# Performance work log

Measured on AMD Instinct MI355X. Metric: run time of the kernel, lower is better.

Reference implementation:

```python
import jax, jax.numpy as jnp
import numpy as np

CFG = {"dt": 1.0, "T_r": 2.0, "kappa_j": 1.0, "tau_j": 10.0, "gamma_m": 1.0, "R_m": 1.0,
       "tau_m": 20.0, "thresh": 1.0, "tau_tr": 20.0, "tau_data": 10.0,
       "alpha_gen": 0.5, "alpha_disc": 0.5}


def _lif(v, x, tr, j, refrac, ti, cfg):
    """One LIF update for a hidden layer (bPC_SNNLayer.update_state)."""
    dt = cfg["dt"]
    j = j + dt / cfg["tau_j"] * (-cfg["kappa_j"] * j + ti)
    is_refr = refrac > 0
    v_next = v + dt / cfg["tau_m"] * (-cfg["gamma_m"] * v + cfg["R_m"] * j)
    v = jnp.where(is_refr, v, v_next)
    spikes = (v > cfg["thresh"]).astype(v.dtype) * (1.0 - is_refr.astype(v.dtype))
    v = v * (1.0 - spikes)
    refrac = jnp.maximum(refrac - dt, 0.0)
    refrac = jnp.where(spikes > 0, jnp.asarray(cfg["T_r"], v.dtype), refrac)
    tr = tr - tr / cfg["tau_tr"] + spikes  # spike trace (layer.x)
    return v, spikes, tr, j, refrac


def _forward(x_data, y_target, W0, W1, W2, V0, V1, V2, num_steps):
    cfg = CFG
    B = x_data.shape[0]
    d0, d1, d2, d3 = x_data.shape[1], W0.shape[1], W1.shape[1], W2.shape[1]
    dt_ = x_data.dtype
    z = lambda d: jnp.zeros((B, d), dt_)
    state = dict(v1=z(d1), tr1=z(d1), j1=z(d1), r1=z(d1), s1=z(d1),
                 v2=z(d2), tr2=z(d2), j2=z(d2), r2=z(d2), s2=z(d2),
                 eg0=z(d0), eg1=z(d1), eg2=z(d2),
                 ed1=z(d1), ed2=z(d2), ed3=z(d3),
                 z_data=z(d0), z_label=z(d3))
    ag, ad = cfg["alpha_gen"], cfg["alpha_disc"]

    def step(st, _):
        # phase 1: currents into hidden layers 1 and 2 (layers 0/3 are data/label, no-op)
        ti1 = -st["eg1"] + st["ed2"] @ V1 - st["ed1"] + st["eg0"] @ W0
        ti2 = -st["eg2"] + st["ed3"] @ V2 - st["ed2"] + st["eg1"] @ W1
        v1, s1, tr1, j1, r1 = _lif(st["v1"], st["tr1"], st["tr1"], st["j1"], st["r1"], ti1, cfg) if False else _lif(st["v1"], st["tr1"], st["tr1"], st["j1"], st["r1"], ti1, cfg)
        v1, s1, tr1, j1, r1 = _lif(st["v1"], st["tr1"], st["tr1"], st["j1"], st["r1"], ti1, cfg)
        v2, s2, tr2, j2, r2 = _lif(st["v2"], st["tr2"], st["tr2"], st["j2"], st["r2"], ti2, cfg)
        # phase 2: error recomputation (training mode with label clamped)
        z_data = st["z_data"] - st["z_data"] / cfg["tau_data"] + x_data
        z_label = st["z_label"] - st["z_label"] / cfg["tau_data"] + y_target
        eg0 = ag * (z_data - s1 @ W0.T)          # layer 0 generative error
        ed1 = ad * (tr1 - x_data @ V0.T)          # layer 1 discriminative error
        eg1 = ag * (tr1 - s2 @ W1.T)
        ed2 = ad * (tr2 - s1 @ V1.T)
        eg2 = ag * (tr2 - y_target @ W2.T)        # top hidden: label-clamped generative target
        ed3 = ad * (z_label - s2 @ V2.T)          # label layer discriminative error
        return dict(v1=v1, tr1=tr1, j1=j1, r1=r1, s1=s1,
                    v2=v2, tr2=tr2, j2=j2, r2=r2, s2=s2,
                    eg0=eg0, eg1=eg1, eg2=eg2, ed1=ed1, ed2=ed2, ed3=ed3,
                    z_data=z_data, z_label=z_label), None

    final, _ = jax.lax.scan(step, state, None, length=num_steps)
    return final["ed3"]


def setup_inputs() -> dict:
    key = jax.random.key(0)
    ks = jax.random.split(key, 8)
    B = 128
    sizes = (2048, 4096, 4096, 512)
    sc = 0.02  # weight scale kept small so dynamics stay numerically sane over 16 steps
    return {
        "x_data": jax.random.normal(ks[0], (B, sizes[0]), jnp.float32),
        "y_target": jax.random.normal(ks[1], (B, sizes[3]), jnp.float32),
        "W0": jax.random.normal(ks[2], (sizes[0], sizes[1]), jnp.float32) * sc,
        "W1": jax.random.normal(ks[3], (sizes[1], sizes[2]), jnp.float32) * sc,
        "W2": jax.random.normal(ks[4], (sizes[2], sizes[3]), jnp.float32) * sc,
        "V0": jax.random.normal(ks[5], (sizes[1], sizes[0]), jnp.float32) * sc,
        "V1": jax.random.normal(ks[6], (sizes[2], sizes[1]), jnp.float32) * sc,
        "V2": jax.random.normal(ks[7], (sizes[3], sizes[2]), jnp.float32) * sc,
        "num_steps": 16,
    }


def reference(x_data, y_target, W0, W1, W2, V0, V1, V2, num_steps):
    return _forward(x_data, y_target, W0, W1, W2, V0, V1, V2, num_steps)
```

## Files before the change

### kernel.cpp

```cpp
#include <hip/hip_runtime.h>


#define DEVINL __device__ __forceinline__

using bf16x8 = __attribute__((ext_vector_type(8))) __bf16;
using f32x4  = __attribute__((ext_vector_type(4))) float;
using i32x4  = __attribute__((ext_vector_type(4))) int;
typedef unsigned char uchar;

static constexpr int BB = 128;
static constexpr int D0 = 2048, D1 = 4096, D2 = 4096, D3 = 512;
static constexpr int NSTEPS = 16;

struct Ctx {
  const float *x, *y, *W0, *W1, *W2, *V0, *V1, *V2;
  float *v1, *j1, *r1, *tr1, *v2, *j2, *r2, *tr2;
  float *zd, *zl, *xV0T, *yW2T;
  __bf16 *x_bf, *y_bf, *eg0_bf, *eg1_bf, *ed2_bf, *ed3_bf;
  uchar *s1_f8, *s2_f8, *WA8, *WB8;
  __bf16 *W0t, *W1t, *V1t, *V2t, *V0n, *W2n;
  float *out;
};

DEVINL void gload16(const void* g, void* l) {
  __builtin_amdgcn_global_load_lds(
      (const __attribute__((address_space(1))) void*)g,
      (__attribute__((address_space(3))) void*)l, 16, 0, 0);
}
DEVINL uint32_t lds_off(const void* p) {
  return (uint32_t)(uintptr_t)(__attribute__((address_space(3))) const void*)p;
}
DEVINL bf16x8 dsr128(uint32_t addr) {
  i32x4 r;
  asm volatile("ds_read_b128 %0, %1" : "=v"(r) : "v"(addr));
  return __builtin_bit_cast(bf16x8, r);
}
DEVINL long dsr64(uint32_t addr) {
  long r;
  asm volatile("ds_read_b64 %0, %1" : "=v"(r) : "v"(addr));
  return r;
}

struct Seg { const __bf16* A; unsigned ldA; const __bf16* W; unsigned ldW; int iters; };
struct SPtr { const __bf16 *a0, *a1, *w; };
struct SPtrW { const __bf16 *a, *w; };

DEVINL SPtr mkptr(const Seg& s, int t) {
  int r = t >> 3;
  int u = ((t & 7) ^ (r & 7)) * 8;
  SPtr p;
  p.a0 = s.A + (size_t)r * s.ldA + u;
  p.a1 = s.A + (size_t)(r + 32) * s.ldA + u;
  p.w  = s.W + (size_t)r * s.ldW + u;
  return p;
}
DEVINL SPtrW mkptrw(const Seg& s, int t) {
  int r = t >> 3;
  int u = ((t & 7) ^ (r & 7)) * 8;
  SPtrW p;
  p.a = s.A + (size_t)r * s.ldA + u;
  p.w = s.W + (size_t)r * s.ldW + u;
  return p;
}

DEVINL void run_gemm(const Seg* segs, int nIter, __bf16* lsA, __bf16* lsW,
                     int t, int wm, int wn, int l16, int lg, f32x4* acc) {
  const int seg0it = segs[0].iters;
  SPtr p = mkptr(segs[0], t);
  int nxt = 0;
  auto stage = [&](int s) {
    __bf16* bA = lsA + (s & 3) * 4096;
    __bf16* bW = lsW + (s & 3) * 2048;
    gload16(p.a0, bA + t * 8);
    gload16(p.a1, bA + 2048 + t * 8);
    gload16(p.w,  bW + t * 8);
    p.a0 += 64; p.a1 += 64; p.w += 64;
    if (++nxt == seg0it) p = mkptr(segs[1], t);
  };

  const int x7 = l16 & 7;
  uint32_t aB = lds_off(lsA), wB = lds_off(lsW);
  uint32_t aAd[2][2], wAd[2];
#pragma unroll
  for (int mt = 0; mt < 2; ++mt)
#pragma unroll
    for (int ks = 0; ks < 2; ++ks)
      aAd[mt][ks] = aB + (uint32_t)(wm * 32 + mt * 16 + l16) * 128u
                       + (uint32_t)(((ks * 4 + lg) ^ x7) * 16);
#pragma unroll
  for (int ks = 0; ks < 2; ++ks)
    wAd[ks] = wB + (uint32_t)(wn * 16 + l16) * 128u
                 + (uint32_t)(((ks * 4 + lg) ^ x7) * 16);

  auto compute = [&](int i) {
    uint32_t oa = (uint32_t)(i & 3) * 8192u, ow = (uint32_t)(i & 3) * 4096u;
    bf16x8 a00 = dsr128(aAd[0][0] + oa);
    bf16x8 a01 = dsr128(aAd[0][1] + oa);
    bf16x8 a10 = dsr128(aAd[1][0] + oa);
    bf16x8 a11 = dsr128(aAd[1][1] + oa);
    bf16x8 b0  = dsr128(wAd[0] + ow);
    bf16x8 b1  = dsr128(wAd[1] + ow);
    asm volatile("s_waitcnt lgkmcnt(0)" ::: "memory");
    __builtin_amdgcn_sched_barrier(0);
    __builtin_amdgcn_s_setprio(1);
    acc[0] = __builtin_amdgcn_mfma_f32_16x16x32_bf16(a00, b0, acc[0], 0, 0, 0);
    acc[1] = __builtin_amdgcn_mfma_f32_16x16x32_bf16(a10, b0, acc[1], 0, 0, 0);
    acc[0] = __builtin_amdgcn_mfma_f32_16x16x32_bf16(a01, b1, acc[0], 0, 0, 0);
    acc[1] = __builtin_amdgcn_mfma_f32_16x16x32_bf16(a11, b1, acc[1], 0, 0, 0);
    __builtin_amdgcn_s_setprio(0);
  };

  stage(0); stage(1); stage(2);
  for (int i = 0; i < nIter - 3; ++i) {
    asm volatile("s_waitcnt vmcnt(6)" ::: "memory");
    __builtin_amdgcn_s_barrier();
    stage(i + 3);
    compute(i);
  }
  asm volatile("s_waitcnt vmcnt(6)" ::: "memory");
  __builtin_amdgcn_s_barrier();
  compute(nIter - 3);
  asm volatile("s_waitcnt vmcnt(3)" ::: "memory");
  __builtin_amdgcn_s_barrier();
  compute(nIter - 2);
  asm volatile("s_waitcnt vmcnt(0)" ::: "memory");
  __builtin_amdgcn_s_barrier();
  compute(nIter - 1);
}

DEVINL void run_gemm128w(const Seg* segs, int nIter, __bf16* lsA, __bf16* lsW,
                         int t, int wm, int wn, int l16, int lg, f32x4* acc) {
  const int seg0it = segs[0].iters;
  SPtrW p = mkptrw(segs[0], t);
  int nxt = 0;
  auto stage = [&](int buf) {
    __bf16* bA = lsA + buf * 8192;
    __bf16* bW = lsW + buf * 8192;
    gload16(p.a,      bA + t * 8);
    gload16(p.a + 64, bA + 4096 + t * 8);
    gload16(p.w,      bW + t * 8);
    gload16(p.w + 64, bW + 4096 + t * 8);
    p.a += 128; p.w += 128;
    if (++nxt == seg0it) p = mkptrw(segs[1], t);
  };

  const int x7 = l16 & 7;
  uint32_t aB = lds_off(lsA), wB = lds_off(lsW);
  uint32_t aAd[2][2], wAd[2];
#pragma unroll
  for (int mt = 0; mt < 2; ++mt)
#pragma unroll
    for (int ks = 0; ks < 2; ++ks)
      aAd[mt][ks] = aB + (uint32_t)(wm * 32 + mt * 16 + l16) * 128u
                       + (uint32_t)(((ks * 4 + lg) ^ x7) * 16);
#pragma unroll
  for (int ks = 0; ks < 2; ++ks)
    wAd[ks] = wB + (uint32_t)(wn * 16 + l16) * 128u
                 + (uint32_t)(((ks * 4 + lg) ^ x7) * 16);

  auto compute = [&](int buf) {
    uint32_t oa = (uint32_t)buf * 16384u, ow = (uint32_t)buf * 16384u;
    bf16x8 a00 = dsr128(aAd[0][0] + oa);
    bf16x8 a01 = dsr128(aAd[0][1] + oa);
    bf16x8 a10 = dsr128(aAd[1][0] + oa);
    bf16x8 a11 = dsr128(aAd[1][1] + oa);
    bf16x8 b0  = dsr128(wAd[0] + ow);
    bf16x8 b1  = dsr128(wAd[1] + ow);
    bf16x8 c00 = dsr128(aAd[0][0] + oa + 8192);
    bf16x8 c01 = dsr128(aAd[0][1] + oa + 8192);
    bf16x8 c10 = dsr128(aAd[1][0] + oa + 8192);
    bf16x8 c11 = dsr128(aAd[1][1] + oa + 8192);
    bf16x8 d0  = dsr128(wAd[0] + ow + 8192);
    bf16x8 d1  = dsr128(wAd[1] + ow + 8192);
    asm volatile("s_waitcnt lgkmcnt(0)" ::: "memory");
    __builtin_amdgcn_sched_barrier(0);
    __builtin_amdgcn_s_setprio(1);
    acc[0] = __builtin_amdgcn_mfma_f32_16x16x32_bf16(a00, b0, acc[0], 0, 0, 0);
    acc[1] = __builtin_amdgcn_mfma_f32_16x16x32_bf16(a10, b0, acc[1], 0, 0, 0);
    acc[0] = __builtin_amdgcn_mfma_f32_16x16x32_bf16(a01, b1, acc[0], 0, 0, 0);
    acc[1] = __builtin_amdgcn_mfma_f32_16x16x32_bf16(a11, b1, acc[1], 0, 0, 0);
    acc[0] = __builtin_amdgcn_mfma_f32_16x16x32_bf16(c00, d0, acc[0], 0, 0, 0);
    acc[1] = __builtin_amdgcn_mfma_f32_16x16x32_bf16(c10, d0, acc[1], 0, 0, 0);
    acc[0] = __builtin_amdgcn_mfma_f32_16x16x32_bf16(c01, d1, acc[0], 0, 0, 0);
    acc[1] = __builtin_amdgcn_mfma_f32_16x16x32_bf16(c11, d1, acc[1], 0, 0, 0);
    __builtin_amdgcn_s_setprio(0);
  };

  stage(0); stage(1);
  int cur = 0, nx = 2;
  for (int i = 0; i < nIter - 2; ++i) {
    asm volatile("s_waitcnt vmcnt(4)" ::: "memory");
    __builtin_amdgcn_s_barrier();
    stage(nx);
    compute(cur);
    cur = (cur == 2) ? 0 : cur + 1;
    nx  = (nx == 2) ? 0 : nx + 1;
  }
  asm volatile("s_waitcnt vmcnt(4)" ::: "memory");
  __builtin_amdgcn_s_barrier();
  compute(cur);
  cur = (cur == 2) ? 0 : cur + 1;
  asm volatile("s_waitcnt vmcnt(0)" ::: "memory");
  __builtin_amdgcn_s_barrier();
  compute(cur);
}


__global__ __launch_bounds__(512, 1) void phase1_v17(Ctx c, float edsc) {
  __shared__ __align__(16) __bf16 lsA[3][8192];
  __shared__ __align__(16) __bf16 lsW[3][8192];
  int t = threadIdx.x, w = t >> 6, l = t & 63;
  int l16 = l & 15, lg = l >> 4, wm = w >> 2, wn = w & 3;
  int bx = blockIdx.x;
  int z = bx >> 7, idx = bx & 127;
  int mh = idx >> 6, n0 = (idx & 63) * 64;
  f32x4 acc[2];
  f32x4 z4 = {0.f, 0.f, 0.f, 0.f};
  acc[0] = z4; acc[1] = z4;

  Seg segs[2]; int nIter, N;
  float *v, *j, *rf, *tr; const float* aux; const __bf16* buf; uchar* sf8;
  if (z == 0) {
    segs[0] = { c.ed2_bf + (size_t)mh * 64 * D2, (unsigned)D2, c.V1t + (size_t)n0 * D2, (unsigned)D2, 32 };
    segs[1] = { c.eg0_bf + (size_t)mh * 64 * D0, (unsigned)D0, c.W0t + (size_t)n0 * D0, (unsigned)D0, 16 };
    nIter = 48; N = D1;
    v = c.v1; j = c.j1; rf = c.r1; tr = c.tr1; buf = c.eg1_bf; aux = c.xV0T; sf8 = c.s1_f8;
  } else {
    segs[0] = { c.ed3_bf + (size_t)mh * 64 * D3, (unsigned)D3, c.V2t + (size_t)n0 * D3, (unsigned)D3, 4 };
    segs[1] = { c.eg1_bf + (size_t)mh * 64 * D1, (unsigned)D1, c.W1t + (size_t)n0 * D1, (unsigned)D1, 32 };
    nIter = 36; N = D2;
    v = c.v2; j = c.j2; rf = c.r2; tr = c.tr2; buf = c.ed2_bf; aux = c.yW2T; sf8 = c.s2_f8;
  }

  run_gemm128w(segs, nIter, &lsA[0][0], &lsW[0][0], t, wm, wn, l16, lg, acc);

  int n = n0 + wn * 16 + l16;
#pragma unroll
  for (int mt = 0; mt < 2; ++mt) {
#pragma unroll
    for (int r = 0; r < 4; ++r) {
      int b = mh * 64 + wm * 32 + mt * 16 + lg * 4 + r;
      size_t idx2 = (size_t)b * N + n;
      float to = tr[idx2];
      float ti = acc[mt][r] - (float)buf[idx2] - edsc * (to - aux[idx2]);
      float jo = j[idx2];
      float jn = jo + 0.1f * (ti - jo);
      float ro = rf[idx2];
      float vo = v[idx2];
      bool refr = ro > 0.0f;
      float vn = refr ? vo : (vo + 0.05f * (jn - vo));
      float sp = (!refr && vn > 1.0f) ? 1.0f : 0.0f;
      if (sp != 0.0f) vn = 0.0f;
      float rn = fmaxf(ro - 1.0f, 0.0f);
      if (sp != 0.0f) rn = 2.0f;
      float tn = to - 0.05f * to + sp;
      v[idx2] = vn; j[idx2] = jn; rf[idx2] = rn; tr[idx2] = tn;
      sf8[idx2] = (sp != 0.0f) ? (uchar)0x38 : (uchar)0;
    }
  }
}


__global__ __launch_bounds__(512, 2) void phase2_v18(Ctx c) {
  __shared__ __align__(128) uchar lsA[4][8192];
  __shared__ __align__(128) uchar lsW[4][8192];
  int t = threadIdx.x, w = t >> 6, l = t & 63;
  int l16 = l & 15, lg = l >> 4, wm = w >> 2, wn = w & 3;
  int g = blockIdx.x, mh = blockIdx.y;

  const uchar *A, *W; int n0; bool isA;
  if (g < 96) { isA = true;  A = c.s1_f8 + (size_t)mh * 64 * D1; W = c.WA8 + (size_t)g * 64 * 4096;        n0 = g * 64; }
  else        { isA = false; A = c.s2_f8 + (size_t)mh * 64 * D2; W = c.WB8 + (size_t)(g - 96) * 64 * 4096; n0 = (g - 96) * 64; }

  f32x4 acc[2];
  f32x4 z4 = {0.f, 0.f, 0.f, 0.f};
  acc[0] = z4; acc[1] = z4;

  int row8 = t >> 3, u8 = t & 7;
  int su8 = (u8 ^ ((row8 >> 1) & 7)) * 16;
  const uchar* pA = A + (size_t)row8 * 4096 + su8;
  const uchar* pW = W + (size_t)row8 * 4096 + su8;
  uchar* dA = &lsA[0][0] + t * 16;
  uchar* dW = &lsW[0][0] + t * 16;
  auto stage = [&](int s) {
    uint32_t o = (uint32_t)(s & 3) * 8192u;
    gload16(pA, dA + o);
    gload16(pW, dW + o);
    pA += 128; pW += 128;
  };

  uint32_t aB = lds_off(lsA), wB = lds_off(lsW);
  uint32_t adA[2], adW;
#pragma unroll
  for (int mt = 0; mt < 2; ++mt) {
    int ra = wm * 32 + mt * 16 + l16;
    adA[mt] = aB + (uint32_t)ra * 128u
            + (uint32_t)((((lg >> 1) ^ ((ra >> 1) & 7)) * 16) + (lg & 1) * 8);
  }
  {
    int rw = wn * 16 + l16;
    adW = wB + (uint32_t)rw * 128u
        + (uint32_t)((((lg >> 1) ^ ((rw >> 1) & 7)) * 16) + (lg & 1) * 8);
  }

  auto compute = [&](int i) {
    uint32_t off = (uint32_t)(i & 3) * 8192u;
    uint32_t A0 = adA[0] + off, A1 = adA[1] + off, B0 = adW + off;
    long a0v0 = dsr64(A0);         long a1v0 = dsr64(A1);
    long b0v0 = dsr64(B0);
    long a0v1 = dsr64(A0 ^ 32u);   long a1v1 = dsr64(A1 ^ 32u);
    long b0v1 = dsr64(B0 ^ 32u);
    long a0v2 = dsr64(A0 ^ 64u);   long a1v2 = dsr64(A1 ^ 64u);
    long b0v2 = dsr64(B0 ^ 64u);
    long a0v3 = dsr64(A0 ^ 96u);   long a1v3 = dsr64(A1 ^ 96u);
    long b0v3 = dsr64(B0 ^ 96u);
    asm volatile("s_waitcnt lgkmcnt(0)" ::: "memory");
    __builtin_amdgcn_sched_barrier(0);
    __builtin_amdgcn_s_setprio(1);
    acc[0] = __builtin_amdgcn_mfma_f32_16x16x32_fp8_fp8(a0v0, b0v0, acc[0], 0, 0, 0);
    acc[1] = __builtin_amdgcn_mfma_f32_16x16x32_fp8_fp8(a1v0, b0v0, acc[1], 0, 0, 0);
    acc[0] = __builtin_amdgcn_mfma_f32_16x16x32_fp8_fp8(a0v1, b0v1, acc[0], 0, 0, 0);
    acc[1] = __builtin_amdgcn_mfma_f32_16x16x32_fp8_fp8(a1v1, b0v1, acc[1], 0, 0, 0);
    acc[0] = __builtin_amdgcn_mfma_f32_16x16x32_fp8_fp8(a0v2, b0v2, acc[0], 0, 0, 0);
    acc[1] = __builtin_amdgcn_mfma_f32_16x16x32_fp8_fp8(a1v2, b0v2, acc[1], 0, 0, 0);
    acc[0] = __builtin_amdgcn_mfma_f32_16x16x32_fp8_fp8(a0v3, b0v3, acc[0], 0, 0, 0);
    acc[1] = __builtin_amdgcn_mfma_f32_16x16x32_fp8_fp8(a1v3, b0v3, acc[1], 0, 0, 0);
    __builtin_amdgcn_s_setprio(0);
  };

  const int nIter = 32;
  stage(0); stage(1); stage(2);
  for (int i = 0; i < nIter - 3; ++i) {
    asm volatile("s_waitcnt vmcnt(4)" ::: "memory");
    __builtin_amdgcn_s_barrier();
    stage(i + 3);
    compute(i);
  }
  asm volatile("s_waitcnt vmcnt(4)" ::: "memory");
  __builtin_amdgcn_s_barrier();
  compute(nIter - 3);
  asm volatile("s_waitcnt vmcnt(2)" ::: "memory");
  __builtin_amdgcn_s_barrier();
  compute(nIter - 2);
  asm volatile("s_waitcnt vmcnt(0)" ::: "memory");
  __builtin_amdgcn_s_barrier();
  compute(nIter - 1);

#pragma unroll
  for (int mt = 0; mt < 2; ++mt) {
    int nn = n0 + wn * 16 + l16;
#pragma unroll
    for (int r = 0; r < 4; ++r) {
      int b = mh * 64 + wm * 32 + mt * 16 + lg * 4 + r;
      float av = acc[mt][r];
      if (isA) {
        if (nn < 2048) {
          size_t idx = (size_t)b * D0 + nn;
          float zo = c.zd[idx]; float zn = zo - 0.1f * zo + c.x[idx];
          c.zd[idx] = zn;
          c.eg0_bf[idx] = (__bf16)(0.5f * (zn - av));
        } else {
          size_t idx = (size_t)b * D2 + (nn - 2048);
          c.ed2_bf[idx] = (__bf16)(0.5f * (c.tr2[idx] - av));
        }
      } else {
        if (nn < 4096) {
          size_t idx = (size_t)b * D1 + nn;
          c.eg1_bf[idx] = (__bf16)(0.5f * (c.tr1[idx] - av));
        } else {
          size_t idx = (size_t)b * D3 + (nn - 4096);
          float zo = c.zl[idx]; float zn = zo - 0.1f * zo + c.y[idx];
          c.zl[idx] = zn;
          float e = 0.5f * (zn - av);
          c.out[idx] = e; c.ed3_bf[idx] = (__bf16)e;
        }
      }
    }
  }
}


__global__ __launch_bounds__(256, 2) void precomp_v6(Ctx c) {
  __shared__ __align__(16) __bf16 lsA[4][4096];
  __shared__ __align__(16) __bf16 lsW[4][2048];
  int t = threadIdx.x, w = t >> 6, l = t & 63;
  int l16 = l & 15, lg = l >> 4, wm = w >> 1, wn = w & 1;
  int n0 = blockIdx.x * 32, mh = blockIdx.y;
  f32x4 acc[2];
  f32x4 z4 = {0.f, 0.f, 0.f, 0.f};
  acc[0] = z4; acc[1] = z4;

  Seg segs[2]; int nIter, N; float* outp;
  if (blockIdx.z == 0) {
    segs[0] = { c.x_bf + (size_t)mh * 64 * D0, (unsigned)D0, c.V0n + (size_t)n0 * D0, (unsigned)D0, 32 };
    nIter = 32; N = D1; outp = c.xV0T;
  } else {
    segs[0] = { c.y_bf + (size_t)mh * 64 * D3, (unsigned)D3, c.W2n + (size_t)n0 * D3, (unsigned)D3, 8 };
    nIter = 8; N = D2; outp = c.yW2T;
  }
  segs[1] = segs[0];

  run_gemm(segs, nIter, &lsA[0][0], &lsW[0][0], t, wm, wn, l16, lg, acc);

  int n = n0 + wn * 16 + l16;
#pragma unroll
  for (int mt = 0; mt < 2; ++mt)
#pragma unroll
    for (int r = 0; r < 4; ++r) {
      int b = mh * 64 + wm * 32 + mt * 16 + lg * 4 + r;
      outp[(size_t)b * N + n] = acc[mt][r];
    }
}


__global__ __launch_bounds__(256) void wprep_kernel(Ctx c, int g0) {
  __shared__ float ls[2][64][65];
  int g = blockIdx.x + g0;
  const float* src; __bf16* tp = nullptr; uchar* n8 = nullptr; __bf16* nb = nullptr; int R, C;
  if (g < 1024)       { src = c.W0; n8 = c.WA8;                         tp = c.W0t; R = D0; C = D1; }
  else if (g < 3072)  { g -= 1024;  src = c.W1; n8 = c.WB8;             tp = c.W1t; R = D1; C = D2; }
  else if (g < 5120)  { g -= 3072;  src = c.V1; n8 = c.WA8 + (size_t)2048 * 4096; tp = c.V1t; R = D2; C = D1; }
  else if (g < 5376)  { g -= 5120;  src = c.V2; n8 = c.WB8 + (size_t)4096 * 4096; tp = c.V2t; R = D3; C = D2; }
  else if (g < 6400)  { g -= 5376;  src = c.V0; nb = c.V0n; R = D1; C = D0; }
  else                { g -= 6400;  src = c.W2; nb = c.W2n; R = D2; C = D3; }
  int tpr = C / 128;
  int r0 = (g / tpr) * 64, c0 = (g % tpr) * 128;
  int t = threadIdx.x, r = t >> 2, q = t & 3;

  const float* base = src + (size_t)(r0 + r) * C + c0 + q * 16;
  float4 vv[2][4];
#pragma unroll
  for (int h = 0; h < 2; ++h)
#pragma unroll
    for (int i = 0; i < 4; ++i)
      vv[h][i] = reinterpret_cast<const float4*>(base + h * 64)[i];

  if (n8) {
#pragma unroll
    for (int h = 0; h < 2; ++h) {
      int pk[4];
#pragma unroll
      for (int i = 0; i < 4; i++) {
        float4 v = vv[h][i];
        ls[h][r][q * 16 + i * 4 + 0] = v.x; ls[h][r][q * 16 + i * 4 + 1] = v.y;
        ls[h][r][q * 16 + i * 4 + 2] = v.z; ls[h][r][q * 16 + i * 4 + 3] = v.w;
        int wd = __builtin_amdgcn_cvt_pk_fp8_f32(v.x, v.y, 0, false);
        wd = __builtin_amdgcn_cvt_pk_fp8_f32(v.z, v.w, wd, true);
        pk[i] = wd;
      }
      int4 pv; pv.x = pk[0]; pv.y = pk[1]; pv.z = pk[2]; pv.w = pk[3];
      *reinterpret_cast<int4*>(n8 + (size_t)(r0 + r) * C + c0 + h * 64 + q * 16) = pv;
    }
    __syncthreads();
#pragma unroll
    for (int h = 0; h < 2; ++h) {
      union { __bf16 hx[16]; int4 qq[2]; } wv;
#pragma unroll
      for (int i = 0; i < 16; i++) wv.hx[i] = (__bf16)ls[h][q * 16 + i][r];
      int4* dt = reinterpret_cast<int4*>(tp + (size_t)(c0 + h * 64 + r) * R + r0 + q * 16);
      dt[0] = wv.qq[0]; dt[1] = wv.qq[1];
    }
  } else {
#pragma unroll
    for (int h = 0; h < 2; ++h) {
      union { __bf16 hx[16]; int4 qq[2]; } uu;
#pragma unroll
      for (int i = 0; i < 4; i++) {
        float4 v = vv[h][i];
        uu.hx[i * 4 + 0] = (__bf16)v.x; uu.hx[i * 4 + 1] = (__bf16)v.y;
        uu.hx[i * 4 + 2] = (__bf16)v.z; uu.hx[i * 4 + 3] = (__bf16)v.w;
      }
      int4* dn = reinterpret_cast<int4*>(nb + (size_t)(r0 + r) * C + c0 + h * 64 + q * 16);
      dn[0] = uu.qq[0]; dn[1] = uu.qq[1];
    }
  }
}

__global__ __launch_bounds__(256) void castinit_kernel(Ctx c) {
  int i = blockIdx.x * 256 + threadIdx.x;
  const int NX = BB * D0 / 4;
  union { __bf16 h[4]; uint2 u; } p, q;
  if (i < NX) {
    float4 xv = reinterpret_cast<const float4*>(c.x)[i];
    reinterpret_cast<float4*>(c.zd)[i] = xv;
    p.h[0] = (__bf16)xv.x; p.h[1] = (__bf16)xv.y; p.h[2] = (__bf16)xv.z; p.h[3] = (__bf16)xv.w;
    reinterpret_cast<uint2*>(c.x_bf)[i] = p.u;
    q.h[0] = (__bf16)(0.5f * xv.x); q.h[1] = (__bf16)(0.5f * xv.y);
    q.h[2] = (__bf16)(0.5f * xv.z); q.h[3] = (__bf16)(0.5f * xv.w);
    reinterpret_cast<uint2*>(c.eg0_bf)[i] = q.u;
  } else {
    int k = i - NX;
    float4 yv = reinterpret_cast<const float4*>(c.y)[k];
    reinterpret_cast<float4*>(c.zl)[k] = yv;
    p.h[0] = (__bf16)yv.x; p.h[1] = (__bf16)yv.y; p.h[2] = (__bf16)yv.z; p.h[3] = (__bf16)yv.w;
    reinterpret_cast<uint2*>(c.y_bf)[k] = p.u;
    q.h[0] = (__bf16)(0.5f * yv.x); q.h[1] = (__bf16)(0.5f * yv.y);
    q.h[2] = (__bf16)(0.5f * yv.z); q.h[3] = (__bf16)(0.5f * yv.w);
    reinterpret_cast<uint2*>(c.ed3_bf)[k] = q.u;
  }
}


extern "C" void kernel_launch(void* const* d_in, const int* in_sizes, int n_in,
                              void* d_out, int out_size, void* d_ws, size_t ws_size,
                              hipStream_t stream) {
  Ctx c;
  c.x  = (const float*)d_in[0];
  c.y  = (const float*)d_in[1];
  c.W0 = (const float*)d_in[2];
  c.W1 = (const float*)d_in[3];
  c.W2 = (const float*)d_in[4];
  c.V0 = (const float*)d_in[5];
  c.V1 = (const float*)d_in[6];
  c.V2 = (const float*)d_in[7];
  c.out = (float*)d_out;

  char* p = (char*)d_ws;
  auto af = [&](size_t n) -> float* { float* r = (float*)p; p += ((n * 4 + 255) & ~(size_t)255); return r; };
  auto ah = [&](size_t n) -> __bf16* { __bf16* r = (__bf16*)p; p += ((n * 2 + 255) & ~(size_t)255); return r; };
  auto au = [&](size_t n) -> uchar* { uchar* r = (uchar*)p; p += ((n + 255) & ~(size_t)255); return r; };

  const size_t S1 = (size_t)BB * D1;
  c.v1 = af(S1); c.j1 = af(S1); c.r1 = af(S1); c.tr1 = af(S1);
  c.v2 = af(S1); c.j2 = af(S1); c.r2 = af(S1); c.tr2 = af(S1);
  c.eg1_bf = ah(S1); c.ed2_bf = ah(S1);
  size_t zero_bytes = (size_t)(p - (char*)d_ws);
  c.zd = af((size_t)BB * D0); c.zl = af((size_t)BB * D3);
  c.xV0T = af(S1); c.yW2T = af(S1);
  c.x_bf = ah((size_t)BB * D0); c.y_bf = ah((size_t)BB * D3);
  c.eg0_bf = ah((size_t)BB * D0); c.ed3_bf = ah((size_t)BB * D3);
  c.s1_f8 = au(S1); c.s2_f8 = au(S1);
  c.W0t = ah((size_t)D0 * D1); c.W1t = ah((size_t)D1 * D2); c.V1t = ah((size_t)D2 * D1); c.V2t = ah((size_t)D3 * D2);
  c.V0n = ah((size_t)D1 * D0); c.W2n = ah((size_t)D2 * D3);
  c.WA8 = au((size_t)(D0 + D2) * 4096);
  c.WB8 = au((size_t)(D1 + D3) * 4096);

  hipMemsetAsync(d_ws, 0, zero_bytes, stream);
  castinit_kernel<<<320, 256, 0, stream>>>(c);
  wprep_kernel<<<1536, 256, 0, stream>>>(c, 5120);
  wprep_kernel<<<2048, 256, 0, stream>>>(c, 1024);
  wprep_kernel<<<2048, 256, 0, stream>>>(c, 3072);
  wprep_kernel<<<1024, 256, 0, stream>>>(c, 0);
  precomp_v6<<<dim3(128, 2, 2), 256, 0, stream>>>(c);

  for (int s = 1; s < NSTEPS; s++) {
    phase1_v17<<<256, 512, 0, stream>>>(c, 0.5f);
    phase2_v18<<<dim3(168, 2), 512, 0, stream>>>(c);
  }
}
```

Measured before the change: 790.8 us.

## Store phase-1 transposed weights as fp8 and upconvert to bf16 in registers

The phase-1 GEMM now streams its transposed weight operands (W0t, W1t, V1t, V2t) as fp8 bytes instead of bf16. The weight-prep kernel writes fp8 transposes, the LDS weight buffer shrinks to bytes, and each wave reads 64-bit chunks and converts them to bf16 before the bf16 MFMAs. This halves weight global-memory traffic and LDS footprint in the memory-bound phase-1 kernel. It adds per-iteration conversion ALU work and loses weight precision, which may change the numerical results.

```diff
diff --git a/kernel.cpp b/kernel.cpp
--- a/kernel.cpp
+++ b/kernel.cpp
@@ -5,6 +5,7 @@
 
 using bf16x8 = __attribute__((ext_vector_type(8))) __bf16;
 using f32x4  = __attribute__((ext_vector_type(4))) float;
+using f32x2  = __attribute__((ext_vector_type(2))) float;
 using i32x4  = __attribute__((ext_vector_type(4))) int;
 typedef unsigned char uchar;
 
@@ -18,7 +19,8 @@
   float *zd, *zl, *xV0T, *yW2T;
   __bf16 *x_bf, *y_bf, *eg0_bf, *eg1_bf, *ed2_bf, *ed3_bf;
   uchar *s1_f8, *s2_f8, *WA8, *WB8;
-  __bf16 *W0t, *W1t, *V1t, *V2t, *V0n, *W2n;
+  uchar *W0t8, *W1t8, *V1t8, *V2t8;
+  __bf16 *V0n, *W2n;
   float *out;
 };
 
@@ -40,10 +42,25 @@
   asm volatile("ds_read_b64 %0, %1" : "=v"(r) : "v"(addr));
   return r;
 }
+DEVINL bf16x8 cvtw(long v) {
+  int lo = (int)(v & 0xffffffffL);
+  int hi = (int)(((unsigned long long)v) >> 32);
+  f32x2 p0 = __builtin_amdgcn_cvt_pk_f32_fp8(lo, false);
+  f32x2 p1 = __builtin_amdgcn_cvt_pk_f32_fp8(lo, true);
+  f32x2 p2 = __builtin_amdgcn_cvt_pk_f32_fp8(hi, false);
+  f32x2 p3 = __builtin_amdgcn_cvt_pk_f32_fp8(hi, true);
+  bf16x8 r;
+  r[0] = (__bf16)p0[0]; r[1] = (__bf16)p0[1];
+  r[2] = (__bf16)p1[0]; r[3] = (__bf16)p1[1];
+  r[4] = (__bf16)p2[0]; r[5] = (__bf16)p2[1];
+  r[6] = (__bf16)p3[0]; r[7] = (__bf16)p3[1];
+  return r;
+}
 
 struct Seg { const __bf16* A; unsigned ldA; const __bf16* W; unsigned ldW; int iters; };
 struct SPtr { const __bf16 *a0, *a1, *w; };
-struct SPtrW { const __bf16 *a, *w; };
+struct Seg8 { const __bf16* A; unsigned ldA; const uchar* W; unsigned ldW; int iters; };
+struct SP8 { const __bf16* a; const uchar* w; };
 
 DEVINL SPtr mkptr(const Seg& s, int t) {
   int r = t >> 3;
@@ -54,12 +71,13 @@
   p.w  = s.W + (size_t)r * s.ldW + u;
   return p;
 }
-DEVINL SPtrW mkptrw(const Seg& s, int t) {
+DEVINL SP8 mkptr8(const Seg8& s, int t) {
   int r = t >> 3;
-  int u = ((t & 7) ^ (r & 7)) * 8;
-  SPtrW p;
-  p.a = s.A + (size_t)r * s.ldA + u;
-  p.w = s.W + (size_t)r * s.ldW + u;
+  int ue = ((t & 7) ^ (r & 7)) * 8;
+  int ub = ((t & 7) ^ (r & 7)) * 16;
+  SP8 p;
+  p.a = s.A + (size_t)r * s.ldA + ue;
+  p.w = s.W + (size_t)r * s.ldW + ub;
   return p;
 }
 
@@ -128,52 +146,62 @@
   compute(nIter - 1);
 }
 
-DEVINL void run_gemm128w(const Seg* segs, int nIter, __bf16* lsA, __bf16* lsW,
-                         int t, int wm, int wn, int l16, int lg, f32x4* acc) {
+DEVINL void run_gemm128w8(const Seg8* segs, int nIter, __bf16* lsA, uchar* lsW8,
+                          int t, int wm, int wn, int l16, int lg, f32x4* acc) {
   const int seg0it = segs[0].iters;
-  SPtrW p = mkptrw(segs[0], t);
+  SP8 p = mkptr8(segs[0], t);
   int nxt = 0;
   auto stage = [&](int buf) {
     __bf16* bA = lsA + buf * 8192;
-    __bf16* bW = lsW + buf * 8192;
+    uchar*  bW = lsW8 + buf * 8192;
     gload16(p.a,      bA + t * 8);
     gload16(p.a + 64, bA + 4096 + t * 8);
-    gload16(p.w,      bW + t * 8);
-    gload16(p.w + 64, bW + 4096 + t * 8);
+    gload16(p.w,      bW + t * 16);
     p.a += 128; p.w += 128;
-    if (++nxt == seg0it) p = mkptrw(segs[1], t);
+    if (++nxt == seg0it) p = mkptr8(segs[1], t);
   };
 
   const int x7 = l16 & 7;
-  uint32_t aB = lds_off(lsA), wB = lds_off(lsW);
-  uint32_t aAd[2][2], wAd[2];
+  uint32_t aB = lds_off(lsA), wB = lds_off(lsW8);
+  uint32_t aAd[2][2], wAd8[2][2];
 #pragma unroll
   for (int mt = 0; mt < 2; ++mt)
 #pragma unroll
     for (int ks = 0; ks < 2; ++ks)
       aAd[mt][ks] = aB + (uint32_t)(wm * 32 + mt * 16 + l16) * 128u
                        + (uint32_t)(((ks * 4 + lg) ^ x7) * 16);
-#pragma unroll
-  for (int ks = 0; ks < 2; ++ks)
-    wAd[ks] = wB + (uint32_t)(wn * 16 + l16) * 128u
-                 + (uint32_t)(((ks * 4 + lg) ^ x7) * 16);
+  {
+    int rw = wn * 16 + l16;
+#pragma unroll
+    for (int h = 0; h < 2; ++h)
+#pragma unroll
+      for (int ks = 0; ks < 2; ++ks) {
+        int j = h * 4 + ks * 2 + (lg >> 1);
+        wAd8[h][ks] = wB + (uint32_t)rw * 128u
+                    + (uint32_t)(((j ^ (rw & 7)) * 16) + (lg & 1) * 8);
+      }
+  }
 
   auto compute = [&](int buf) {
-    uint32_t oa = (uint32_t)buf * 16384u, ow = (uint32_t)buf * 16384u;
+    uint32_t oa = (uint32_t)buf * 16384u, ow = (uint32_t)buf * 8192u;
     bf16x8 a00 = dsr128(aAd[0][0] + oa);
     bf16x8 a01 = dsr128(aAd[0][1] + oa);
     bf16x8 a10 = dsr128(aAd[1][0] + oa);
     bf16x8 a11 = dsr128(aAd[1][1] + oa);
-    bf16x8 b0  = dsr128(wAd[0] + ow);
-    bf16x8 b1  = dsr128(wAd[1] + ow);
     bf16x8 c00 = dsr128(aAd[0][0] + oa + 8192);
     bf16x8 c01 = dsr128(aAd[0][1] + oa + 8192);
     bf16x8 c10 = dsr128(aAd[1][0] + oa + 8192);
     bf16x8 c11 = dsr128(aAd[1][1] + oa + 8192);
-    bf16x8 d0  = dsr128(wAd[0] + ow + 8192);
-    bf16x8 d1  = dsr128(wAd[1] + ow + 8192);
+    long w00 = dsr64(wAd8[0][0] + ow);
+    long w01 = dsr64(wAd8[0][1] + ow);
+    long w10 = dsr64(wAd8[1][0] + ow);
+    long w11 = dsr64(wAd8[1][1] + ow);
     asm volatile("s_waitcnt lgkmcnt(0)" ::: "memory");
     __builtin_amdgcn_sched_barrier(0);
+    bf16x8 b0 = cvtw(w00);
+    bf16x8 b1 = cvtw(w01);
+    bf16x8 d0 = cvtw(w10);
+    bf16x8 d1 = cvtw(w11);
     __builtin_amdgcn_s_setprio(1);
     acc[0] = __builtin_amdgcn_mfma_f32_16x16x32_bf16(a00, b0, acc[0], 0, 0, 0);
     acc[1] = __builtin_amdgcn_mfma_f32_16x16x32_bf16(a10, b0, acc[1], 0, 0, 0);
@@ -189,14 +217,14 @@
   stage(0); stage(1);
   int cur = 0, nx = 2;
   for (int i = 0; i < nIter - 2; ++i) {
-    asm volatile("s_waitcnt vmcnt(4)" ::: "memory");
+    asm volatile("s_waitcnt vmcnt(3)" ::: "memory");
     __builtin_amdgcn_s_barrier();
     stage(nx);
     compute(cur);
     cur = (cur == 2) ? 0 : cur + 1;
     nx  = (nx == 2) ? 0 : nx + 1;
   }
-  asm volatile("s_waitcnt vmcnt(4)" ::: "memory");
+  asm volatile("s_waitcnt vmcnt(3)" ::: "memory");
   __builtin_amdgcn_s_barrier();
   compute(cur);
   cur = (cur == 2) ? 0 : cur + 1;
@@ -206,9 +234,9 @@
 }
 
 
-__global__ __launch_bounds__(512, 1) void phase1_v17(Ctx c, float edsc) {
+__global__ __launch_bounds__(512, 1) void phase1_v21(Ctx c, float edsc) {
   __shared__ __align__(16) __bf16 lsA[3][8192];
-  __shared__ __align__(16) __bf16 lsW[3][8192];
+  __shared__ __align__(128) uchar lsW8[3][8192];
   int t = threadIdx.x, w = t >> 6, l = t & 63;
   int l16 = l & 15, lg = l >> 4, wm = w >> 2, wn = w & 3;
   int bx = blockIdx.x;
@@ -218,21 +246,21 @@
   f32x4 z4 = {0.f, 0.f, 0.f, 0.f};
   acc[0] = z4; acc[1] = z4;
 
-  Seg segs[2]; int nIter, N;
+  Seg8 segs[2]; int nIter, N;
   float *v, *j, *rf, *tr; const float* aux; const __bf16* buf; uchar* sf8;
   if (z == 0) {
-    segs[0] = { c.ed2_bf + (size_t)mh * 64 * D2, (unsigned)D2, c.V1t + (size_t)n0 * D2, (unsigned)D2, 32 };
-    segs[1] = { c.eg0_bf + (size_t)mh * 64 * D0, (unsigned)D0, c.W0t + (size_t)n0 * D0, (unsigned)D0, 16 };
+    segs[0] = { c.ed2_bf + (size_t)mh * 64 * D2, (unsigned)D2, c.V1t8 + (size_t)n0 * D2, (unsigned)D2, 32 };
+    segs[1] = { c.eg0_bf + (size_t)mh * 64 * D0, (unsigned)D0, c.W0t8 + (size_t)n0 * D0, (unsigned)D0, 16 };
     nIter = 48; N = D1;
     v = c.v1; j = c.j1; rf = c.r1; tr = c.tr1; buf = c.eg1_bf; aux = c.xV0T; sf8 = c.s1_f8;
   } else {
-    segs[0] = { c.ed3_bf + (size_t)mh * 64 * D3, (unsigned)D3, c.V2t + (size_t)n0 * D3, (unsigned)D3, 4 };
-    segs[1] = { c.eg1_bf + (size_t)mh * 64 * D1, (unsigned)D1, c.W1t + (size_t)n0 * D1, (unsigned)D1, 32 };
+    segs[0] = { c.ed3_bf + (size_t)mh * 64 * D3, (unsigned)D3, c.V2t8 + (size_t)n0 * D3, (unsigned)D3, 4 };
+    segs[1] = { c.eg1_bf + (size_t)mh * 64 * D1, (unsigned)D1, c.W1t8 + (size_t)n0 * D1, (unsigned)D1, 32 };
     nIter = 36; N = D2;
     v = c.v2; j = c.j2; rf = c.r2; tr = c.tr2; buf = c.ed2_bf; aux = c.yW2T; sf8 = c.s2_f8;
   }
 
-  run_gemm128w(segs, nIter, &lsA[0][0], &lsW[0][0], t, wm, wn, l16, lg, acc);
+  run_gemm128w8(segs, nIter, &lsA[0][0], &lsW8[0][0], t, wm, wn, l16, lg, acc);
 
   int n = n0 + wn * 16 + l16;
 #pragma unroll
@@ -416,11 +444,11 @@
 __global__ __launch_bounds__(256) void wprep_kernel(Ctx c, int g0) {
   __shared__ float ls[2][64][65];
   int g = blockIdx.x + g0;
-  const float* src; __bf16* tp = nullptr; uchar* n8 = nullptr; __bf16* nb = nullptr; int R, C;
-  if (g < 1024)       { src = c.W0; n8 = c.WA8;                         tp = c.W0t; R = D0; C = D1; }
-  else if (g < 3072)  { g -= 1024;  src = c.W1; n8 = c.WB8;             tp = c.W1t; R = D1; C = D2; }
-  else if (g < 5120)  { g -= 3072;  src = c.V1; n8 = c.WA8 + (size_t)2048 * 4096; tp = c.V1t; R = D2; C = D1; }
-  else if (g < 5376)  { g -= 5120;  src = c.V2; n8 = c.WB8 + (size_t)4096 * 4096; tp = c.V2t; R = D3; C = D2; }
+  const float* src; uchar* t8 = nullptr; uchar* n8 = nullptr; __bf16* nb = nullptr; int R, C;
+  if (g < 1024)       { src = c.W0; n8 = c.WA8;                         t8 = c.W0t8; R = D0; C = D1; }
+  else if (g < 3072)  { g -= 1024;  src = c.W1; n8 = c.WB8;             t8 = c.W1t8; R = D1; C = D2; }
+  else if (g < 5120)  { g -= 3072;  src = c.V1; n8 = c.WA8 + (size_t)2048 * 4096; t8 = c.V1t8; R = D2; C = D1; }
+  else if (g < 5376)  { g -= 5120;  src = c.V2; n8 = c.WB8 + (size_t)4096 * 4096; t8 = c.V2t8; R = D3; C = D2; }
   else if (g < 6400)  { g -= 5376;  src = c.V0; nb = c.V0n; R = D1; C = D0; }
   else                { g -= 6400;  src = c.W2; nb = c.W2n; R = D2; C = D3; }
   int tpr = C / 128;
@@ -454,11 +482,19 @@
     __syncthreads();
 #pragma unroll
     for (int h = 0; h < 2; ++h) {
-      union { __bf16 hx[16]; int4 qq[2]; } wv;
-#pragma unroll
-      for (int i = 0; i < 16; i++) wv.hx[i] = (__bf16)ls[h][q * 16 + i][r];
-      int4* dt = reinterpret_cast<int4*>(tp + (size_t)(c0 + h * 64 + r) * R + r0 + q * 16);
-      dt[0] = wv.qq[0]; dt[1] = wv.qq[1];
+      int pk[4];
+#pragma unroll
+      for (int i = 0; i < 4; i++) {
+        float f0 = ls[h][q * 16 + i * 4 + 0][r];
+        float f1 = ls[h][q * 16 + i * 4 + 1][r];
+        float f2 = ls[h][q * 16 + i * 4 + 2][r];
+        float f3 = ls[h][q * 16 + i * 4 + 3][r];
+        int wd = __builtin_amdgcn_cvt_pk_fp8_f32(f0, f1, 0, false);
+        wd = __builtin_amdgcn_cvt_pk_fp8_f32(f2, f3, wd, true);
+        pk[i] = wd;
+      }
+      int4 pv; pv.x = pk[0]; pv.y = pk[1]; pv.z = pk[2]; pv.w = pk[3];
+      *reinterpret_cast<int4*>(t8 + (size_t)(c0 + h * 64 + r) * R + r0 + q * 16) = pv;
     }
   } else {
 #pragma unroll
@@ -530,7 +566,8 @@
   c.x_bf = ah((size_t)BB * D0); c.y_bf = ah((size_t)BB * D3);
   c.eg0_bf = ah((size_t)BB * D0); c.ed3_bf = ah((size_t)BB * D3);
   c.s1_f8 = au(S1); c.s2_f8 = au(S1);
-  c.W0t = ah((size_t)D0 * D1); c.W1t = ah((size_t)D1 * D2); c.V1t = ah((size_t)D2 * D1); c.V2t = ah((size_t)D3 * D2);
+  c.W0t8 = au((size_t)D1 * D0); c.W1t8 = au((size_t)D2 * D1);
+  c.V1t8 = au((size_t)D1 * D2); c.V2t8 = au((size_t)D2 * D3);
   c.V0n = ah((size_t)D1 * D0); c.W2n = ah((size_t)D2 * D3);
   c.WA8 = au((size_t)(D0 + D2) * 4096);
   c.WB8 = au((size_t)(D1 + D3) * 4096);
@@ -544,7 +581,7 @@
   precomp_v6<<<dim3(128, 2, 2), 256, 0, stream>>>(c);
 
   for (int s = 1; s < NSTEPS; s++) {
-    phase1_v17<<<256, 512, 0, stream>>>(c, 0.5f);
+    phase1_v21<<<256, 512, 0, stream>>>(c, 0.5f);
     phase2_v18<<<dim3(168, 2), 512, 0, stream>>>(c);
   }
 }
```

Measured after the change: 816.7 us. 3.3% more time.
